# Kernel tuning notes

Measured on AMD Instinct MI355X. Metric: run time of the kernel, lower is better.

Reference implementation:

```python
import jax, jax.numpy as jnp
import numpy as np

EMB_DIM = 256
HEAD_DIM = 32


def setup_inputs() -> dict:
    key = jax.random.key(0)
    kx, kq, kk, kv = jax.random.split(key, 4)
    B, S = 4, 4096
    x = jax.random.normal(kx, (B, S, EMB_DIM), dtype=jnp.float32)
    # Linear(emb_dim, head_dim, bias=False): store as [emb_dim, head_dim]
    sc = 1.0 / np.sqrt(EMB_DIM)
    Wq = jax.random.normal(kq, (EMB_DIM, HEAD_DIM), dtype=jnp.float32) * sc
    Wk = jax.random.normal(kk, (EMB_DIM, HEAD_DIM), dtype=jnp.float32) * sc
    Wv = jax.random.normal(kv, (EMB_DIM, HEAD_DIM), dtype=jnp.float32) * sc
    return {"x": x, "Wq": Wq, "Wk": Wk, "Wv": Wv}


def reference(x, Wq, Wk, Wv):
    # single-head attention with POST-softmax scaling (as in source).
    # Dropout treated as identity (eval mode) for determinism.
    scaling = HEAD_DIM ** (-0.5)
    q = jnp.einsum('bse,ed->bsd', x, Wq)
    k = jnp.einsum('bse,ed->bsd', x, Wk)
    v = jnp.einsum('bse,ed->bsd', x, Wv)
    energy = jnp.einsum('bqd,bkd->bqk', q, k)  # [B,S,S]
    att = jax.nn.softmax(energy, axis=-1) * scaling
    out = jnp.einsum('bqk,bkd->bqd', att, v)
    return out
```

## Files before the change

kernel.cpp:

```cpp
#include <hip/hip_runtime.h>

#define EMB 256
#define HD 32
#define SEQ 4096
#define NSPLIT 8
#define KRANGE 512
#define NT (KRANGE / 32)
#define NQROW 16384

typedef _Float16 half8 __attribute__((ext_vector_type(8)));
typedef _Float16 half4v __attribute__((ext_vector_type(4)));
typedef _Float16 half2v __attribute__((ext_vector_type(2)));
typedef float floatx4 __attribute__((ext_vector_type(4)));
typedef float floatx16 __attribute__((ext_vector_type(16)));
typedef unsigned uint2v __attribute__((ext_vector_type(2)));

#define L2E 1.44269504088896340736f
#define SCALING 0.17677669529663687f
#define DEFER_THR 8.0f

__device__ __forceinline__ half8 mk8(unsigned a, unsigned b, unsigned c, unsigned d) {
  union { unsigned u[4]; half8 h; } z;
  z.u[0] = a; z.u[1] = b; z.u[2] = c; z.u[3] = d;
  return z.h;
}

__device__ __forceinline__ void plswap(unsigned& a, unsigned& b) {
#if __has_builtin(__builtin_amdgcn_permlane32_swap)
  uint2v r = __builtin_amdgcn_permlane32_swap(a, b, false, false);
  a = r[0]; b = r[1];
#else
  unsigned sa = (unsigned)__shfl_xor((int)a, 32);
  unsigned sb = (unsigned)__shfl_xor((int)b, 32);
  bool hi = (threadIdx.x & 32) != 0;
  unsigned na = hi ? sb : a;
  unsigned nb = hi ? b : sa;
  a = na; b = nb;
#endif
}

__device__ __forceinline__ float sum2(unsigned pk, float acc) {
  half2v a = __builtin_bit_cast(half2v, pk);
#if __has_builtin(__builtin_amdgcn_fdot2)
  half2v one; one[0] = (_Float16)1.f; one[1] = (_Float16)1.f;
  return __builtin_amdgcn_fdot2(a, one, acc, false);
#else
  return acc + (float)a[0] + (float)a[1];
#endif
}

__global__ __launch_bounds__(256) void qkv_kernel(const float* __restrict__ x,
                                                  const float* __restrict__ Wq,
                                                  const float* __restrict__ Wk,
                                                  const float* __restrict__ Wv,
                                                  _Float16* __restrict__ qw,
                                                  _Float16* __restrict__ kw,
                                                  _Float16* __restrict__ vt2) {
  __shared__ _Float16 wsl[24576];
  const int tid = threadIdx.x;

#pragma unroll
  for (int i = 0; i < 24; ++i) {
    const float* W = (i < 8) ? Wq : ((i < 16) ? Wk : Wv);
    int lu = (i & 7) * 1024 + tid * 4;
    float4 v4 = *(const float4*)(W + lu);
    int e = lu >> 5;
    int d0 = lu & 31;
    int kc = e >> 5, quad = (e >> 3) & 3, j = e & 7;
    int half = d0 >> 4;
    int n0 = d0 & 15;
    int mat = i >> 3;
    int base = (((mat * 2 + half) * 8 + kc) << 9) + (quad << 7) + j;
    float sc = (i < 8) ? L2E : 1.f;
    wsl[base + (n0 + 0) * 8] = (_Float16)(v4.x * sc);
    wsl[base + (n0 + 1) * 8] = (_Float16)(v4.y * sc);
    wsl[base + (n0 + 2) * 8] = (_Float16)(v4.z * sc);
    wsl[base + (n0 + 3) * 8] = (_Float16)(v4.w * sc);
  }
  __syncthreads();

  int lane = tid & 63, wave = tid >> 6;
  int n = lane & 15, quad = lane >> 4;
  int rowbase = blockIdx.x * 64 + wave * 16;

  floatx4 cq0 = {0,0,0,0}, cq1 = {0,0,0,0};
  floatx4 ck0 = {0,0,0,0}, ck1 = {0,0,0,0};
  floatx4 cv0 = {0,0,0,0}, cv1 = {0,0,0,0};

#pragma unroll
  for (int kc = 0; kc < 8; ++kc) {
    const float* xp = x + (size_t)(rowbase + n) * EMB + kc * 32 + quad * 8;
    float4 xa = *(const float4*)(xp);
    float4 xb = *(const float4*)(xp + 4);
    half8 a;
    a[0] = (_Float16)xa.x; a[1] = (_Float16)xa.y; a[2] = (_Float16)xa.z; a[3] = (_Float16)xa.w;
    a[4] = (_Float16)xb.x; a[5] = (_Float16)xb.y; a[6] = (_Float16)xb.z; a[7] = (_Float16)xb.w;
    const _Float16* wp = wsl + (kc << 9) + (lane << 3);
    half8 bq0 = *(const half8*)(wp);
    half8 bq1 = *(const half8*)(wp + (8  << 9));
    half8 bk0 = *(const half8*)(wp + (16 << 9));
    half8 bk1 = *(const half8*)(wp + (24 << 9));
    half8 bv0 = *(const half8*)(wp + (32 << 9));
    half8 bv1 = *(const half8*)(wp + (40 << 9));
    cq0 = __builtin_amdgcn_mfma_f32_16x16x32_f16(a, bq0, cq0, 0, 0, 0);
    cq1 = __builtin_amdgcn_mfma_f32_16x16x32_f16(a, bq1, cq1, 0, 0, 0);
    ck0 = __builtin_amdgcn_mfma_f32_16x16x32_f16(a, bk0, ck0, 0, 0, 0);
    ck1 = __builtin_amdgcn_mfma_f32_16x16x32_f16(a, bk1, ck1, 0, 0, 0);
    cv0 = __builtin_amdgcn_mfma_f32_16x16x32_f16(a, bv0, cv0, 0, 0, 0);
    cv1 = __builtin_amdgcn_mfma_f32_16x16x32_f16(a, bv1, cv1, 0, 0, 0);
  }

  int b = rowbase >> 12;
  int s0 = rowbase & (SEQ - 1);
  _Float16* vbase = vt2 + (size_t)b * SEQ * HD;
#pragma unroll
  for (int r = 0; r < 4; ++r) {
    int row = rowbase + quad * 4 + r;
    qw[row * HD + n]      = (_Float16)cq0[r];
    qw[row * HD + n + 16] = (_Float16)cq1[r];
    kw[row * HD + n]      = (_Float16)ck0[r];
    kw[row * HD + n + 16] = (_Float16)ck1[r];
    int s = s0 + quad * 4 + r;
    int blk = (s >> 3) << 8, sl = s & 7;
    vbase[blk + n * 8 + sl]        = (_Float16)cv0[r];
    vbase[blk + (n + 16) * 8 + sl] = (_Float16)cv1[r];
  }
}

__global__ __launch_bounds__(256, 4) void attn_kernel(const _Float16* __restrict__ q,
                                                      const _Float16* __restrict__ k,
                                                      const _Float16* __restrict__ vt2,
                                                      _Float16* __restrict__ Op,
                                                      float* __restrict__ Mp,
                                                      float* __restrict__ Lp) {
  const int t = threadIdx.x;
  const int w = t >> 6, lane = t & 63;
  const int n2 = lane & 31, h = lane >> 5;
  const int qb = blockIdx.x & 127;
  const int sp = blockIdx.x >> 7;
  const int b = qb >> 5;
  const int qrow0 = qb * 128 + w * 32;
  const int key0 = sp * KRANGE;

  const _Float16* kb = k   + (size_t)(b * SEQ + key0) * HD;
  const _Float16* vb = vt2 + (size_t)b * SEQ * HD + (size_t)key0 * HD;

  half8 qf0 = *(const half8*)(q + (qrow0 + n2) * HD + h * 8);
  half8 qf1 = *(const half8*)(q + (qrow0 + n2) * HD + 16 + h * 8);

  floatx16 o;
#pragma unroll
  for (int r = 0; r < 16; ++r) o[r] = 0.f;
  const floatx16 zero16 = o;
  float m = -__builtin_huge_valf();
  float mtrue = -__builtin_huge_valf();
  float l = 0.f;

  auto ldt = [&](int tile, half8& k0, half8& k1, half8& v0, half8& v1) {
    const _Float16* kn = kb + (size_t)(tile * 32 + n2) * HD;
    const _Float16* vn = vb + tile * 1024;
    k0 = *(const half8*)(kn + h * 8);
    k1 = *(const half8*)(kn + 16 + h * 8);
    v0 = *(const half8*)(vn + h * 256 + n2 * 8);
    v1 = *(const half8*)(vn + 512 + h * 256 + n2 * 8);
  };

  auto tilecomp = [&](half8 tka0, half8 tka1, half8 tva0, half8 tva1) {
    floatx16 s = __builtin_amdgcn_mfma_f32_32x32x16_f16(tka0, qf0, zero16, 0, 0, 0);
    s = __builtin_amdgcn_mfma_f32_32x32x16_f16(tka1, qf1, s, 0, 0, 0);

    floatx4 s0 = {s[0], s[1], s[2], s[3]};
    floatx4 s1 = {s[4], s[5], s[6], s[7]};
    floatx4 s2 = {s[8], s[9], s[10], s[11]};
    floatx4 s3 = {s[12], s[13], s[14], s[15]};
    floatx4 t01 = __builtin_elementwise_max(s0, s1);
    floatx4 t23 = __builtin_elementwise_max(s2, s3);
    floatx4 t4  = __builtin_elementwise_max(t01, t23);
    float mm = fmaxf(fmaxf(t4[0], t4[1]), fmaxf(t4[2], t4[3]));
    mm = fmaxf(mm, __shfl_xor(mm, 32));
    mtrue = fmaxf(mtrue, mm);

    if (__any(mm > m + DEFER_THR)) {
      float mnew = fmaxf(m, mm);
      float alpha = __builtin_amdgcn_exp2f(m - mnew);
      m = mnew;
#pragma unroll
      for (int r = 0; r < 16; ++r) o[r] *= alpha;
      l *= alpha;
    }

    unsigned pk[8];
#pragma unroll
    for (int g = 0; g < 8; ++g) {
      float p0 = __builtin_amdgcn_exp2f(s[2 * g] - m);
      float p1 = __builtin_amdgcn_exp2f(s[2 * g + 1] - m);
      pk[g] = __builtin_bit_cast(unsigned, __builtin_amdgcn_cvt_pkrtz(p0, p1));
    }

    float lA = sum2(pk[3], sum2(pk[2], sum2(pk[1], sum2(pk[0], 0.f))));
    float lB = sum2(pk[7], sum2(pk[6], sum2(pk[5], sum2(pk[4], 0.f))));
    l += lA + lB;

    unsigned b00 = pk[0], b02 = pk[2]; plswap(b00, b02);
    unsigned b01 = pk[1], b03 = pk[3]; plswap(b01, b03);
    unsigned b10 = pk[4], b12 = pk[6]; plswap(b10, b12);
    unsigned b11 = pk[5], b13 = pk[7]; plswap(b11, b13);

    o = __builtin_amdgcn_mfma_f32_32x32x16_f16(tva0, mk8(b00, b01, b02, b03), o, 0, 0, 0);
    o = __builtin_amdgcn_mfma_f32_32x32x16_f16(tva1, mk8(b10, b11, b12, b13), o, 0, 0, 0);
  };

  half8 ak0, ak1, av0, av1, bk0, bk1, bv0, bv1;
  ldt(0, ak0, ak1, av0, av1);
  ldt(1, bk0, bk1, bv0, bv1);

#pragma unroll
  for (int kt = 0; kt < NT; kt += 2) {
    half8 ck0, ck1, cv0, cv1, dk0, dk1, dv0, dv1;
    ldt((kt + 2) & (NT - 1), ck0, ck1, cv0, cv1);
    tilecomp(ak0, ak1, av0, av1);
    ldt((kt + 3) & (NT - 1), dk0, dk1, dv0, dv1);
    tilecomp(bk0, bk1, bv0, bv1);
    ak0 = ck0; ak1 = ck1; av0 = cv0; av1 = cv1;
    bk0 = dk0; bk1 = dk1; bv0 = dv0; bv1 = dv1;
  }

  float scale = __builtin_amdgcn_exp2f(m - mtrue);
  l *= scale;
  l = l + __shfl_xor(l, 32);

  size_t obase = ((size_t)(sp * NQROW + qrow0) + n2) * 32;
#pragma unroll
  for (int bb = 0; bb < 4; ++bb) {
    half4v pv;
    pv[0] = (_Float16)(o[4 * bb + 0] * scale);
    pv[1] = (_Float16)(o[4 * bb + 1] * scale);
    pv[2] = (_Float16)(o[4 * bb + 2] * scale);
    pv[3] = (_Float16)(o[4 * bb + 3] * scale);
    *(half4v*)&Op[obase + 8 * bb + 4 * h] = pv;
  }
  if (h == 0) {
    int mi = sp * NQROW + qrow0 + n2;
    Mp[mi] = mtrue;
    Lp[mi] = l;
  }
}

__global__ __launch_bounds__(256) void combine_kernel(const _Float16* __restrict__ Op,
                                                      const float* __restrict__ Mp,
                                                      const float* __restrict__ Lp,
                                                      float* __restrict__ out) {
  int gid = blockIdx.x * 256 + threadIdx.x;
  int dc = gid & 7, qrow = gid >> 3;
  float mv[NSPLIT];
  float ms = -__builtin_huge_valf();
#pragma unroll
  for (int sp = 0; sp < NSPLIT; ++sp) {
    mv[sp] = Mp[sp * NQROW + qrow];
    ms = fmaxf(ms, mv[sp]);
  }
  float L = 0.f;
  floatx4 O = {0.f, 0.f, 0.f, 0.f};
#pragma unroll
  for (int sp = 0; sp < NSPLIT; ++sp) {
    float ww = __builtin_amdgcn_exp2f(mv[sp] - ms);
    L += ww * Lp[sp * NQROW + qrow];
    half4v ov = *(const half4v*)&Op[((size_t)(sp * NQROW + qrow)) * 32 + dc * 4];
#pragma unroll
    for (int r = 0; r < 4; ++r) O[r] += ww * (float)ov[r];
  }
  float inv = SCALING / L;
  floatx4 res = {O[0] * inv, O[1] * inv, O[2] * inv, O[3] * inv};
  *(floatx4*)&out[qrow * HD + dc * 4] = res;
}

extern "C" void kernel_launch(void* const* d_in, const int* in_sizes, int n_in,
                              void* d_out, int out_size, void* d_ws, size_t ws_size,
                              hipStream_t stream) {
  const float* x  = (const float*)d_in[0];
  const float* Wq = (const float*)d_in[1];
  const float* Wk = (const float*)d_in[2];
  const float* Wv = (const float*)d_in[3];
  float* out = (float*)d_out;

  _Float16* qw  = (_Float16*)d_ws;
  _Float16* kw  = qw + NQROW * HD;
  _Float16* vt2 = kw + NQROW * HD;
  _Float16* Op  = vt2 + NQROW * HD;
  float* Mp = (float*)(Op + (size_t)NSPLIT * NQROW * 32);
  float* Lp = Mp + NSPLIT * NQROW;

  qkv_kernel<<<256, 256, 0, stream>>>(x, Wq, Wk, Wv, qw, kw, vt2);
  attn_kernel<<<1024, 256, 0, stream>>>(qw, kw, vt2, Op, Mp, Lp);
  combine_kernel<<<512, 256, 0, stream>>>(Op, Mp, Lp, out);
}
```

Measured before the change: 95.96 us.

## Fuse split-K combine into attention kernel via intra-block LDS reduction

Restructures the attention kernel so each 512-thread block handles 32 query rows, and each of its 8 waves processes a different 512-key split. Partial outputs, maxima and sums go to shared memory and are combined in-block, which removes the separate combine kernel and the global round trip for partials. In exchange each block carries more LDS and a barrier, the number of blocks halves, and the launch-bounds change could alter register allocation and occupancy.

```diff
diff --git a/kernel.cpp b/kernel.cpp
--- a/kernel.cpp
+++ b/kernel.cpp
@@ -127,20 +127,20 @@
   }
 }
 
-__global__ __launch_bounds__(256, 4) void attn_kernel(const _Float16* __restrict__ q,
+__global__ __launch_bounds__(512, 4) void attn_kernel(const _Float16* __restrict__ q,
                                                       const _Float16* __restrict__ k,
                                                       const _Float16* __restrict__ vt2,
-                                                      _Float16* __restrict__ Op,
-                                                      float* __restrict__ Mp,
-                                                      float* __restrict__ Lp) {
+                                                      float* __restrict__ out) {
+  __shared__ float sO[NSPLIT * 32 * 36];
+  __shared__ float sM[NSPLIT * 32];
+  __shared__ float sL[NSPLIT * 32];
+
   const int t = threadIdx.x;
   const int w = t >> 6, lane = t & 63;
   const int n2 = lane & 31, h = lane >> 5;
-  const int qb = blockIdx.x & 127;
-  const int sp = blockIdx.x >> 7;
-  const int b = qb >> 5;
-  const int qrow0 = qb * 128 + w * 32;
-  const int key0 = sp * KRANGE;
+  const int qrow0 = blockIdx.x * 32;
+  const int b = qrow0 >> 12;
+  const int key0 = w * KRANGE;
 
   const _Float16* kb = k   + (size_t)(b * SEQ + key0) * HD;
   const _Float16* vb = vt2 + (size_t)b * SEQ * HD + (size_t)key0 * HD;
@@ -229,49 +229,38 @@
   l *= scale;
   l = l + __shfl_xor(l, 32);
 
-  size_t obase = ((size_t)(sp * NQROW + qrow0) + n2) * 32;
 #pragma unroll
   for (int bb = 0; bb < 4; ++bb) {
-    half4v pv;
-    pv[0] = (_Float16)(o[4 * bb + 0] * scale);
-    pv[1] = (_Float16)(o[4 * bb + 1] * scale);
-    pv[2] = (_Float16)(o[4 * bb + 2] * scale);
-    pv[3] = (_Float16)(o[4 * bb + 3] * scale);
-    *(half4v*)&Op[obase + 8 * bb + 4 * h] = pv;
+    floatx4 pv = {o[4 * bb + 0] * scale, o[4 * bb + 1] * scale,
+                  o[4 * bb + 2] * scale, o[4 * bb + 3] * scale};
+    *(floatx4*)&sO[w * 1152 + n2 * 36 + 8 * bb + 4 * h] = pv;
   }
   if (h == 0) {
-    int mi = sp * NQROW + qrow0 + n2;
-    Mp[mi] = mtrue;
-    Lp[mi] = l;
-  }
-}
-
-__global__ __launch_bounds__(256) void combine_kernel(const _Float16* __restrict__ Op,
-                                                      const float* __restrict__ Mp,
-                                                      const float* __restrict__ Lp,
-                                                      float* __restrict__ out) {
-  int gid = blockIdx.x * 256 + threadIdx.x;
-  int dc = gid & 7, qrow = gid >> 3;
-  float mv[NSPLIT];
-  float ms = -__builtin_huge_valf();
-#pragma unroll
-  for (int sp = 0; sp < NSPLIT; ++sp) {
-    mv[sp] = Mp[sp * NQROW + qrow];
-    ms = fmaxf(ms, mv[sp]);
-  }
-  float L = 0.f;
-  floatx4 O = {0.f, 0.f, 0.f, 0.f};
-#pragma unroll
-  for (int sp = 0; sp < NSPLIT; ++sp) {
-    float ww = __builtin_amdgcn_exp2f(mv[sp] - ms);
-    L += ww * Lp[sp * NQROW + qrow];
-    half4v ov = *(const half4v*)&Op[((size_t)(sp * NQROW + qrow)) * 32 + dc * 4];
-#pragma unroll
-    for (int r = 0; r < 4; ++r) O[r] += ww * (float)ov[r];
-  }
-  float inv = SCALING / L;
-  floatx4 res = {O[0] * inv, O[1] * inv, O[2] * inv, O[3] * inv};
-  *(floatx4*)&out[qrow * HD + dc * 4] = res;
+    sM[w * 32 + n2] = mtrue;
+    sL[w * 32 + n2] = l;
+  }
+  __syncthreads();
+
+#pragma unroll
+  for (int it = 0; it < 2; ++it) {
+    int idx = it * 512 + t;
+    int qr = idx >> 5, d = idx & 31;
+    float mv[NSPLIT];
+    float ms = -__builtin_huge_valf();
+#pragma unroll
+    for (int w2 = 0; w2 < NSPLIT; ++w2) {
+      mv[w2] = sM[w2 * 32 + qr];
+      ms = fmaxf(ms, mv[w2]);
+    }
+    float L = 0.f, O = 0.f;
+#pragma unroll
+    for (int w2 = 0; w2 < NSPLIT; ++w2) {
+      float ww = __builtin_amdgcn_exp2f(mv[w2] - ms);
+      L += ww * sL[w2 * 32 + qr];
+      O += ww * sO[w2 * 1152 + qr * 36 + d];
+    }
+    out[(size_t)(qrow0 + qr) * HD + d] = O * SCALING / L;
+  }
 }
 
 extern "C" void kernel_launch(void* const* d_in, const int* in_sizes, int n_in,
@@ -286,11 +275,7 @@
   _Float16* qw  = (_Float16*)d_ws;
   _Float16* kw  = qw + NQROW * HD;
   _Float16* vt2 = kw + NQROW * HD;
-  _Float16* Op  = vt2 + NQROW * HD;
-  float* Mp = (float*)(Op + (size_t)NSPLIT * NQROW * 32);
-  float* Lp = Mp + NSPLIT * NQROW;
 
   qkv_kernel<<<256, 256, 0, stream>>>(x, Wq, Wk, Wv, qw, kw, vt2);
-  attn_kernel<<<1024, 256, 0, stream>>>(qw, kw, vt2, Op, Mp, Lp);
-  combine_kernel<<<512, 256, 0, stream>>>(Op, Mp, Lp, out);
-}
+  attn_kernel<<<512, 512, 0, stream>>>(qw, kw, vt2, out);
+}
```

Measured after the change: 93.20 us. 1.03x faster.
